# Kernel optimization log

Hardware: AMD Instinct MI355X
Metric: run time of the kernel (lower is better)

Reference implementation:

```python
import jax, jax.numpy as jnp
import numpy as np

D_EMBED = 2048
N_HEAD = 16
HEAD_DIM = D_EMBED // N_HEAD
B, S = 4, 2048


def setup_inputs() -> dict:
    key = jax.random.key(0)
    ks = jax.random.split(key, 6)
    s = 0.02
    x = jax.random.normal(ks[0], (B, S, D_EMBED), dtype=jnp.float32)
    attention_mask = jnp.ones((B, S), dtype=bool)
    Wq = jax.random.normal(ks[1], (D_EMBED, D_EMBED), dtype=jnp.float32) * s
    Wk = jax.random.normal(ks[2], (D_EMBED, D_EMBED), dtype=jnp.float32) * s
    Wv = jax.random.normal(ks[3], (D_EMBED, D_EMBED), dtype=jnp.float32) * s
    Wo = jax.random.normal(ks[4], (D_EMBED, D_EMBED), dtype=jnp.float32) * s
    bq = jnp.zeros((D_EMBED,), jnp.float32)
    bk = jnp.zeros((D_EMBED,), jnp.float32)
    bv = jnp.zeros((D_EMBED,), jnp.float32)
    bo = jnp.zeros((D_EMBED,), jnp.float32)
    return {"x": x, "attention_mask": attention_mask,
            "Wq": Wq, "bq": bq, "Wk": Wk, "bk": bk,
            "Wv": Wv, "bv": bv, "Wo": Wo, "bo": bo}


def reference(x, attention_mask, Wq, bq, Wk, bk, Wv, bv, Wo, bo):
    bsz, seq_len, _ = x.shape

    def split_heads(t):  # [B,S,D] -> [B,H,S,hd]
        return t.reshape(bsz, seq_len, N_HEAD, HEAD_DIM).transpose(0, 2, 1, 3)

    q = split_heads(x @ Wq + bq)
    k = split_heads(x @ Wk + bk)
    v = split_heads(x @ Wv + bv)

    scale = 1.0 / np.sqrt(HEAD_DIM).astype(np.float32)
    scores = jnp.einsum('bhqd,bhkd->bhqk', q, k) * scale  # [B,H,S,S]

    # causal (past_len = 0, query_len = total_len = S) combined with key padding mask
    causal = jnp.tril(jnp.ones((seq_len, seq_len), dtype=bool))  # [S,S]
    mask = causal[None, None, :, :] & attention_mask[:, None, None, :]
    neg = jnp.finfo(scores.dtype).min
    scores = jnp.where(mask, scores, neg)

    att = jax.nn.softmax(scores, axis=-1)  # dropout p=0.0 -> identity
    out = jnp.einsum('bhqk,bhkd->bhqd', att, v)
    out = out.transpose(0, 2, 1, 3).reshape(bsz, seq_len, D_EMBED)
    return out @ Wo + bo
```

## Files before the change

kernel.cpp:

```cpp
#include <hip/hip_runtime.h>
#include <cstdint>
#include <cstddef>


#define D_EMBED 2048
#define NHEAD   16
#define HDIM    128
#define BATCH   4
#define SEQ     2048
#define MROWS   (BATCH*SEQ)

typedef __attribute__((ext_vector_type(8))) short bf16x8;
typedef __attribute__((ext_vector_type(4))) float f32x4;

__device__ __forceinline__ short f2bf(float f) {
  union { float f; uint32_t u; } v; v.f = f;
  uint32_t r = v.u + 0x7fffu + ((v.u >> 16) & 1u);
  return (short)(r >> 16);
}

__device__ __forceinline__ void async_copy16(void* lds, const void* gmem) {
  __builtin_amdgcn_global_load_lds(
      (__attribute__((address_space(1))) void*)gmem,
      (__attribute__((address_space(3))) void*)lds, 16, 0, 0);
}

__global__ __launch_bounds__(256) void cvt_x(const float* __restrict__ x,
                                             short* __restrict__ xb) {
  int i = blockIdx.x * 256 + threadIdx.x;
  float4 v = reinterpret_cast<const float4*>(x)[i];
  short4 o;
  o.x = f2bf(v.x); o.y = f2bf(v.y); o.z = f2bf(v.z); o.w = f2bf(v.w);
  reinterpret_cast<short4*>(xb)[i] = o;
}

struct TransArgs { const float* src[4]; short* dst[4]; };

__global__ __launch_bounds__(256) void transpose_w(TransArgs ta) {
  const int z = blockIdx.z;
  const float* W = ta.src[z];
  short* Wt = ta.dst[z];
  __shared__ float tile[32][33];
  int bx = blockIdx.x * 32, by = blockIdx.y * 32;
  int tx = threadIdx.x & 31, ty = threadIdx.x >> 5;
#pragma unroll
  for (int r = ty; r < 32; r += 8)
    tile[r][tx] = W[(size_t)(by + r) * D_EMBED + bx + tx];
  __syncthreads();
#pragma unroll
  for (int r = ty; r < 32; r += 8)
    Wt[(size_t)(bx + r) * D_EMBED + by + tx] = f2bf(tile[tx][r]);
}

struct GemmArgs {
  const short* A;
  const short* Bt[3];
  const float* bias[3];
  void*        out[3];
  float        scale[3];
  int          mode[3];
};

__global__ __launch_bounds__(512, 2) void gemm256(GemmArgs ga) {
  const int z = blockIdx.z;
  const short* __restrict__ A  = ga.A;
  const short* __restrict__ Bt = ga.Bt[z];

  const int lin  = blockIdx.y * 8 + blockIdx.x;
  const int wg   = (lin & 7) * 32 + (lin >> 3);
  const int col0 = (wg & 7) * 256;
  const int row0 = (wg >> 3) * 256;

  __shared__ __align__(16) short As[2][2][2][64 * 64];
  __shared__ __align__(16) short Bs[2][2][128 * 64];

  const int tid  = threadIdx.x;
  const int lane = tid & 63, w = tid >> 6;
  const int lr   = lane & 15, quad = lane >> 4;
  const int wm   = w >> 2, wn = w & 3;
  const int lr8  = lane >> 3;
  const int srccol = ((lane & 7) ^ ((lane >> 3) & 7)) * 8;
  const int csw = (quad ^ (lr & 7)) * 8;

  bf16x8 av[4][2], bva[2][2], bvb[2][2];
  f32x4 acc[8][4] = {};

#define STAGE_A(buf, Mh, kk) do {                                              \
    _Pragma("unroll")                                                          \
    for (int j = 0; j < 2; ++j)                                                \
      async_copy16(&As[buf][Mh][j][w * 512],                                   \
          A + (size_t)(row0 + j * 128 + (Mh) * 64 + w * 8 + lr8) * D_EMBED +   \
              (kk) + srccol);                                                  \
  } while (0)

#define STAGE_B(buf, Nh, kk) do {                                              \
    _Pragma("unroll")                                                          \
    for (int j = 0; j < 2; ++j) {                                              \
      int fr_ = j * 64 + w * 8 + lr8;                                          \
      async_copy16(&Bs[buf][Nh][(j * 64 + w * 8) * 64],                        \
          Bt + (size_t)(col0 + (fr_ >> 5) * 64 + (Nh) * 32 + (fr_ & 31)) *     \
                  D_EMBED + (kk) + srccol);                                    \
    }                                                                          \
  } while (0)

#define LOAD_A(buf, Mh) do {                                                   \
    _Pragma("unroll")                                                          \
    for (int t = 0; t < 4; ++t) {                                              \
      const short* ap_ = &As[buf][Mh][wm][(t * 16 + lr) * 64];                 \
      av[t][0] = *reinterpret_cast<const bf16x8*>(ap_ + csw);                  \
      av[t][1] = *reinterpret_cast<const bf16x8*>(ap_ + (csw ^ 32));           \
    }                                                                          \
  } while (0)

#define LOAD_B(buf, Nh, dst) do {                                              \
    _Pragma("unroll")                                                          \
    for (int u = 0; u < 2; ++u) {                                              \
      const short* bp_ = &Bs[buf][Nh][(wn * 32 + u * 16 + lr) * 64];           \
      dst[u][0] = *reinterpret_cast<const bf16x8*>(bp_ + csw);                 \
      dst[u][1] = *reinterpret_cast<const bf16x8*>(bp_ + (csw ^ 32));          \
    }                                                                          \
  } while (0)

#define MFMA_Q(Mh, Nh, bv) do {                                                \
    _Pragma("unroll")                                                          \
    for (int ks = 0; ks < 2; ++ks)                                             \
      _Pragma("unroll")                                                        \
      for (int t = 0; t < 4; ++t)                                              \
        _Pragma("unroll")                                                      \
        for (int u = 0; u < 2; ++u)                                            \
          acc[(Mh) * 4 + t][(Nh) * 2 + u] =                                    \
              __builtin_amdgcn_mfma_f32_16x16x32_bf16(                         \
                  av[t][ks], bv[u][ks], acc[(Mh) * 4 + t][(Nh) * 2 + u],       \
                  0, 0, 0);                                                    \
  } while (0)

#define PHASE(Mh, Nh, bv) do {                                                 \
    __builtin_amdgcn_s_setprio(1);                                             \
    MFMA_Q(Mh, Nh, bv);                                                        \
    __builtin_amdgcn_s_setprio(0);                                             \
    __builtin_amdgcn_s_barrier();                                              \
  } while (0)

  STAGE_A(0, 0, 0);  STAGE_B(0, 0, 0);  STAGE_B(0, 1, 0);  STAGE_A(0, 1, 0);
  STAGE_A(1, 0, 64); STAGE_B(1, 0, 64); STAGE_B(1, 1, 64); STAGE_A(1, 1, 64);
  asm volatile("s_waitcnt vmcnt(0)" ::: "memory");
  __builtin_amdgcn_s_barrier();
  LOAD_B(0, 0, bva);

#pragma unroll 1
  for (int it = 0; it < 16; ++it) {
    const int kc = it * 128;
    LOAD_A(0, 0); LOAD_B(0, 1, bvb);
    PHASE(0, 0, bva);
    STAGE_A(0, 0, kc + 128); STAGE_B(0, 0, kc + 128);
    PHASE(0, 1, bvb);
    LOAD_A(0, 1);
    STAGE_B(0, 1, kc + 128);
    PHASE(1, 1, bvb);
    LOAD_B(1, 0, bvb);
    STAGE_A(0, 1, kc + 128);
    asm volatile("s_waitcnt vmcnt(4)" ::: "memory");
    PHASE(1, 0, bva);
    LOAD_A(1, 0); LOAD_B(1, 1, bva);
    PHASE(0, 0, bvb);
    STAGE_B(1, 0, kc + 192); STAGE_A(1, 0, kc + 192);
    PHASE(0, 1, bva);
    LOAD_A(1, 1);
    STAGE_B(1, 1, kc + 192);
    PHASE(1, 1, bva);
    LOAD_B(0, 0, bva);
    STAGE_A(1, 1, kc + 192);
    asm volatile("s_waitcnt vmcnt(4)" ::: "memory");
    PHASE(1, 0, bvb);
  }
  asm volatile("s_waitcnt vmcnt(0)" ::: "memory");

#undef STAGE_A
#undef STAGE_B
#undef LOAD_A
#undef LOAD_B
#undef MFMA_Q
#undef PHASE

  const float* __restrict__ bias = ga.bias[z];
  const int mode = ga.mode[z];
  const float scl = ga.scale[z];
  if (mode != 2) {
#pragma unroll
    for (int mi = 0; mi < 8; ++mi)
#pragma unroll
      for (int ni = 0; ni < 4; ++ni) {
        int n = col0 + wn * 64 + ni * 16 + lr;
        float bias_n = bias[n];
#pragma unroll
        for (int i = 0; i < 4; ++i) {
          int m = row0 + wm * 128 + mi * 16 + quad * 4 + i;
          float v = (acc[mi][ni][i] + bias_n) * scl;
          if (mode == 0) ((short*)ga.out[z])[(size_t)m * D_EMBED + n] = f2bf(v);
          else           ((float*)ga.out[z])[(size_t)m * D_EMBED + n] = v;
        }
      }
  } else {
    short* Vt = (short*)ga.out[z];
#pragma unroll
    for (int ni = 0; ni < 4; ++ni) {
      int n = col0 + wn * 64 + ni * 16 + lr;
      int h = n >> 7, dd = n & (HDIM - 1);
      float bias_n = bias[n];
#pragma unroll
      for (int mi = 0; mi < 8; ++mi)
#pragma unroll
        for (int i = 0; i < 4; ++i) {
          int m = row0 + wm * 128 + mi * 16 + quad * 4 + i;
          int b = m >> 11, t = m & (SEQ - 1);
          Vt[(size_t)((b * NHEAD + h) * HDIM + dd) * SEQ + t] = f2bf(acc[mi][ni][i] + bias_n);
        }
    }
  }
}

#define COMPUTE_STRIP(Kp, Vp, qf, o, l_i, qrow, diag, t0)                       \
  {                                                                             \
    f32x4 sc[4] = {};                                                           \
    __builtin_amdgcn_s_setprio(1);                                              \
    _Pragma("unroll")                                                           \
    for (int nt = 0; nt < 4; ++nt)                                              \
      _Pragma("unroll")                                                         \
      for (int ks = 0; ks < 4; ++ks) {                                          \
        bf16x8 kf = *reinterpret_cast<const bf16x8*>(                           \
            &(Kp)[(nt * 16 + lr) * 128 + (((ks * 4 + quad) ^ lr) * 8)]);        \
        sc[nt] = __builtin_amdgcn_mfma_f32_16x16x32_bf16(qf[ks], kf, sc[nt], 0, 0, 0); \
      }                                                                         \
    __builtin_amdgcn_s_setprio(0);                                              \
    if (diag) {                                                                 \
      _Pragma("unroll")                                                         \
      for (int nt = 0; nt < 4; ++nt) {                                          \
        int t = (t0) + nt * 16 + lr;                                            \
        _Pragma("unroll")                                                       \
        for (int i = 0; i < 4; ++i)                                             \
          if (t > (qrow) + quad * 4 + i) sc[nt][i] = -1e30f;                    \
      }                                                                         \
    }                                                                           \
    _Pragma("unroll")                                                           \
    for (int nt = 0; nt < 4; ++nt)                                              \
      _Pragma("unroll")                                                         \
      for (int i = 0; i < 4; ++i) {                                             \
        float p = exp2f(sc[nt][i]);                                             \
        l_i[i] += p;                                                            \
        Pls[wave][(quad * 4 + i) * 72 + nt * 16 + lr] = f2bf(p);                \
      }                                                                         \
    __builtin_amdgcn_s_setprio(1);                                              \
    _Pragma("unroll")                                                           \
    for (int n2 = 0; n2 < 8; ++n2)                                              \
      _Pragma("unroll")                                                         \
      for (int k2 = 0; k2 < 2; ++k2) {                                          \
        bf16x8 pf = *reinterpret_cast<const bf16x8*>(                           \
            &Pls[wave][lr * 72 + k2 * 32 + quad * 8]);                          \
        bf16x8 vf = *reinterpret_cast<const bf16x8*>(                           \
            &(Vp)[(n2 * 16 + lr) * 64 + (((k2 * 4 + quad) ^ (lr & 7)) * 8)]);   \
        o[n2] = __builtin_amdgcn_mfma_f32_16x16x32_bf16(pf, vf, o[n2], 0, 0, 0);\
      }                                                                         \
    __builtin_amdgcn_s_setprio(0);                                              \
  }

#define FINALIZE_STRIP(o, l_i, qrow)                                            \
  {                                                                             \
    _Pragma("unroll")                                                           \
    for (int off = 1; off < 16; off <<= 1)                                      \
      _Pragma("unroll")                                                         \
      for (int i = 0; i < 4; ++i) l_i[i] += __shfl_xor(l_i[i], off);            \
    float inv_l[4];                                                             \
    _Pragma("unroll")                                                           \
    for (int i = 0; i < 4; ++i) inv_l[i] = 1.0f / l_i[i];                       \
    short* obase = O + (size_t)(b * SEQ + (qrow)) * D_EMBED + h * HDIM;         \
    _Pragma("unroll")                                                           \
    for (int n2 = 0; n2 < 8; ++n2)                                              \
      _Pragma("unroll")                                                         \
      for (int i = 0; i < 4; ++i)                                               \
        obase[(size_t)(quad * 4 + i) * D_EMBED + n2 * 16 + lr] =                \
            f2bf(o[n2][i] * inv_l[i]);                                          \
  }

#define STAGE_KV(cb, tbase)                                                     \
  {                                                                             \
    _Pragma("unroll")                                                           \
    for (int s = 0; s < 4; ++s) {                                               \
      int r0 = wave * 16 + s * 4;                                               \
      int r  = r0 + krow;                                                       \
      int cg = (kcg_base ^ ((s * 4 + krow) & 15)) * 8;                          \
      async_copy16(&Kls[cb][r0 * 128],                                          \
                   Kbase + (size_t)((tbase) + r) * D_EMBED + cg);               \
    }                                                                           \
    _Pragma("unroll")                                                           \
    for (int s = 0; s < 4; ++s) {                                               \
      int r0 = wave * 32 + s * 8;                                               \
      int r  = r0 + vrow;                                                       \
      async_copy16(&Vls[cb][r0 * 64],                                           \
                   Vtbase + (size_t)r * SEQ + (tbase) + vcg);                   \
    }                                                                           \
  }

__global__ __launch_bounds__(256, 2) void flash_attn(const short* __restrict__ Q,
                                                     const short* __restrict__ K,
                                                     const short* __restrict__ Vt,
                                                     short* __restrict__ O) {
  __shared__ short Kls[2][64 * 128];
  __shared__ short Vls[2][128 * 64];
  __shared__ short Pls[4][16 * 72];

  const int lane = threadIdx.x & 63, wave = threadIdx.x >> 6;
  const int lr = lane & 15, quad = lane >> 4;
  const int b = blockIdx.z, h = blockIdx.y;
  const int qb_lo = blockIdx.x;
  const int qb_hi = 31 - qb_lo;
  const int qrow_lo = qb_lo * 64 + wave * 16;
  const int qrow_hi = qb_hi * 64 + wave * 16;

  const int krow = lane >> 4;
  const int kcg_base = lane & 15;
  const int vrow = lane >> 3;
  const int vcg = ((lane & 7) ^ (lane >> 3)) * 8;

  bf16x8 qf_lo[4], qf_hi[4];
  {
    const short* qp0 = Q + (size_t)(b * SEQ + qrow_lo + lr) * D_EMBED + h * HDIM;
    const short* qp1 = Q + (size_t)(b * SEQ + qrow_hi + lr) * D_EMBED + h * HDIM;
#pragma unroll
    for (int ks = 0; ks < 4; ++ks) {
      qf_lo[ks] = *reinterpret_cast<const bf16x8*>(qp0 + ks * 32 + quad * 8);
      qf_hi[ks] = *reinterpret_cast<const bf16x8*>(qp1 + ks * 32 + quad * 8);
    }
  }

  f32x4 o_lo[8] = {}, o_hi[8] = {};
  float l_lo[4] = {}, l_hi[4] = {};

  const short* Kbase  = K + (size_t)b * SEQ * D_EMBED + h * HDIM;
  const short* Vtbase = Vt + (size_t)((b * NHEAD + h) * HDIM) * SEQ;

  STAGE_KV(0, 0);
  __syncthreads();

  int cur = 0;
  for (int tt = 0; tt <= qb_hi; ++tt) {
    const int t0 = tt * 64;
    if (tt < qb_hi) STAGE_KV(cur ^ 1, t0 + 64);
    const short* Kp = &Kls[cur][0];
    const short* Vp = &Vls[cur][0];

    COMPUTE_STRIP(Kp, Vp, qf_hi, o_hi, l_hi, qrow_hi, tt == qb_hi, t0);
    if (tt <= qb_lo)
      COMPUTE_STRIP(Kp, Vp, qf_lo, o_lo, l_lo, qrow_lo, tt == qb_lo, t0);

    __syncthreads();
    cur ^= 1;
  }

  FINALIZE_STRIP(o_hi, l_hi, qrow_hi);
  FINALIZE_STRIP(o_lo, l_lo, qrow_lo);
}

extern "C" void kernel_launch(void* const* d_in, const int* in_sizes, int n_in,
                              void* d_out, int out_size, void* d_ws, size_t ws_size,
                              hipStream_t stream) {
  const float* x  = (const float*)d_in[0];
  const float* Wq = (const float*)d_in[2];
  const float* bq = (const float*)d_in[3];
  const float* Wk = (const float*)d_in[4];
  const float* bk = (const float*)d_in[5];
  const float* Wv = (const float*)d_in[6];
  const float* bv = (const float*)d_in[7];
  const float* Wo = (const float*)d_in[8];
  const float* bo = (const float*)d_in[9];

  char* ws = (char*)d_ws;
  const size_t MB32 = (size_t)MROWS * D_EMBED * 2;
  const size_t WSZ  = (size_t)D_EMBED * D_EMBED * 2;
  short* Xb   = (short*)(ws);
  short* Wqt  = (short*)(ws + MB32);
  short* Wkt  = (short*)(ws + MB32 + WSZ);
  short* Wvt  = (short*)(ws + MB32 + 2 * WSZ);
  short* Wot  = (short*)(ws + MB32 + 3 * WSZ);
  short* Qb   = (short*)(ws + 2 * MB32);
  short* Kb   = (short*)(ws + 3 * MB32);
  short* Vtb  = (short*)(ws + 4 * MB32);
  short* attn = Xb;

  const float scale2 = 0.08838834764831845f * 1.4426950408889634f;

  cvt_x<<<(MROWS * D_EMBED) / 4 / 256, 256, 0, stream>>>(x, Xb);

  TransArgs ta{{Wq, Wk, Wv, Wo}, {Wqt, Wkt, Wvt, Wot}};
  transpose_w<<<dim3(64, 64, 4), 256, 0, stream>>>(ta);

  GemmArgs ga;
  ga.A = Xb;
  ga.Bt[0] = Wqt; ga.Bt[1] = Wkt; ga.Bt[2] = Wvt;
  ga.bias[0] = bq; ga.bias[1] = bk; ga.bias[2] = bv;
  ga.out[0] = Qb; ga.out[1] = Kb; ga.out[2] = Vtb;
  ga.scale[0] = scale2; ga.scale[1] = 1.f; ga.scale[2] = 1.f;
  ga.mode[0] = 0; ga.mode[1] = 0; ga.mode[2] = 2;
  gemm256<<<dim3(D_EMBED / 256, MROWS / 256, 3), 512, 0, stream>>>(ga);

  flash_attn<<<dim3(16, NHEAD, BATCH), 256, 0, stream>>>(Qb, Kb, Vtb, attn);

  GemmArgs gb;
  gb.A = attn;
  gb.Bt[0] = Wot; gb.Bt[1] = Wot; gb.Bt[2] = Wot;
  gb.bias[0] = bo; gb.bias[1] = bo; gb.bias[2] = bo;
  gb.out[0] = d_out; gb.out[1] = d_out; gb.out[2] = d_out;
  gb.scale[0] = 1.f; gb.scale[1] = 1.f; gb.scale[2] = 1.f;
  gb.mode[0] = 1; gb.mode[1] = 1; gb.mode[2] = 1;
  gemm256<<<dim3(D_EMBED / 256, MROWS / 256, 1), 512, 0, stream>>>(gb);
}
```

Before: 583.2 us.

## Software-pipeline flash attention: compute next tile's QK before current PV

Splits the per-tile attention step into separate QK, softmax and PV pieces and reorders them. Each iteration now runs softmax on scores computed in the previous iteration, issues the next tile's QK MFMAs, then does PV for the current tile. K is staged two tiles ahead and V one tile ahead, so exp/convert work can overlap with matrix instructions and loads land earlier. The cost is more live score registers and a more complex prologue with its own wait and barriers, which could lower occupancy.

```diff
diff --git a/kernel.cpp b/kernel.cpp
--- a/kernel.cpp
+++ b/kernel.cpp
@@ -219,9 +219,10 @@
   }
 }
 
-#define COMPUTE_STRIP(Kp, Vp, qf, o, l_i, qrow, diag, t0)                       \
-  {                                                                             \
-    f32x4 sc[4] = {};                                                           \
+#define QK_ONE(Kp, qf, sc)                                                      \
+  {                                                                             \
+    _Pragma("unroll")                                                           \
+    for (int nt = 0; nt < 4; ++nt) sc[nt] = (f32x4){0.f, 0.f, 0.f, 0.f};        \
     __builtin_amdgcn_s_setprio(1);                                              \
     _Pragma("unroll")                                                           \
     for (int nt = 0; nt < 4; ++nt)                                              \
@@ -232,6 +233,10 @@
         sc[nt] = __builtin_amdgcn_mfma_f32_16x16x32_bf16(qf[ks], kf, sc[nt], 0, 0, 0); \
       }                                                                         \
     __builtin_amdgcn_s_setprio(0);                                              \
+  }
+
+#define SM_ONE(sc, l_i, qrow, diag, t0)                                         \
+  {                                                                             \
     if (diag) {                                                                 \
       _Pragma("unroll")                                                         \
       for (int nt = 0; nt < 4; ++nt) {                                          \
@@ -249,6 +254,10 @@
         l_i[i] += p;                                                            \
         Pls[wave][(quad * 4 + i) * 72 + nt * 16 + lr] = f2bf(p);                \
       }                                                                         \
+  }
+
+#define PV_ONE(Vp, o)                                                           \
+  {                                                                             \
     __builtin_amdgcn_s_setprio(1);                                              \
     _Pragma("unroll")                                                           \
     for (int n2 = 0; n2 < 8; ++n2)                                              \
@@ -281,7 +290,7 @@
             f2bf(o[n2][i] * inv_l[i]);                                          \
   }
 
-#define STAGE_KV(cb, tbase)                                                     \
+#define STAGE_K(cb, tbase)                                                      \
   {                                                                             \
     _Pragma("unroll")                                                           \
     for (int s = 0; s < 4; ++s) {                                               \
@@ -291,6 +300,10 @@
       async_copy16(&Kls[cb][r0 * 128],                                          \
                    Kbase + (size_t)((tbase) + r) * D_EMBED + cg);               \
     }                                                                           \
+  }
+
+#define STAGE_V(cb, tbase)                                                      \
+  {                                                                             \
     _Pragma("unroll")                                                           \
     for (int s = 0; s < 4; ++s) {                                               \
       int r0 = wave * 32 + s * 8;                                               \
@@ -338,22 +351,32 @@
   const short* Kbase  = K + (size_t)b * SEQ * D_EMBED + h * HDIM;
   const short* Vtbase = Vt + (size_t)((b * NHEAD + h) * HDIM) * SEQ;
 
-  STAGE_KV(0, 0);
-  __syncthreads();
-
-  int cur = 0;
+  STAGE_K(0, 0); STAGE_V(0, 0); STAGE_K(1, 64);
+  asm volatile("s_waitcnt vmcnt(0)" ::: "memory");
+  __builtin_amdgcn_s_barrier();
+
+  f32x4 sc_hi[4], sc_lo[4];
+  QK_ONE(&Kls[0][0], qf_hi, sc_hi);
+  QK_ONE(&Kls[0][0], qf_lo, sc_lo);
+  __builtin_amdgcn_s_barrier();
+
   for (int tt = 0; tt <= qb_hi; ++tt) {
     const int t0 = tt * 64;
-    if (tt < qb_hi) STAGE_KV(cur ^ 1, t0 + 64);
-    const short* Kp = &Kls[cur][0];
-    const short* Vp = &Vls[cur][0];
-
-    COMPUTE_STRIP(Kp, Vp, qf_hi, o_hi, l_hi, qrow_hi, tt == qb_hi, t0);
-    if (tt <= qb_lo)
-      COMPUTE_STRIP(Kp, Vp, qf_lo, o_lo, l_lo, qrow_lo, tt == qb_lo, t0);
+    const int nxt = (tt + 1) & 1;
+    if (tt + 2 <= qb_hi) STAGE_K(tt & 1, t0 + 128);
+    if (tt + 1 <= qb_hi) STAGE_V(nxt, t0 + 64);
+
+    SM_ONE(sc_hi, l_hi, qrow_hi, tt == qb_hi, t0);
+    if (tt + 1 <= qb_hi) QK_ONE(&Kls[nxt][0], qf_hi, sc_hi);
+    PV_ONE(&Vls[tt & 1][0], o_hi);
+
+    if (tt <= qb_lo) {
+      SM_ONE(sc_lo, l_lo, qrow_lo, tt == qb_lo, t0);
+      if (tt + 1 <= qb_lo) QK_ONE(&Kls[nxt][0], qf_lo, sc_lo);
+      PV_ONE(&Vls[tt & 1][0], o_lo);
+    }
 
     __syncthreads();
-    cur ^= 1;
   }
 
   FINALIZE_STRIP(o_hi, l_hi, qrow_hi);
```

New measurement: 577.7 us. About the same (-0.9%).
